# Kernel tuning notes

Hardware: AMD Instinct MI355X
Metric: run time of the kernel (lower is better)

Reference implementation:

```python
import jax, jax.numpy as jnp
import numpy as np

T, B, IN, H1, HB = 512, 256, 64, 128, 32  # seq, batch, input, LSTM width, bottleneck


def _lstm(x, w_ih, w_hh, b_ih, b_hh):
    """Single-layer unidirectional LSTM, time-major x: [T,B,in] -> [T,B,H].
    PyTorch gate order: i, f, g, o. Zero initial state."""
    H = w_hh.shape[1]
    # hoist input projection out of the scan: [T,B,4H]
    xg = jnp.einsum('tbi,gi->tbg', x, w_ih) + b_ih + b_hh

    def step(carry, xt):
        h, c = carry
        g = xt + h @ w_hh.T
        i, f, gg, o = jnp.split(g, 4, axis=-1)
        c = jax.nn.sigmoid(f) * c + jax.nn.sigmoid(i) * jnp.tanh(gg)
        h = jax.nn.sigmoid(o) * jnp.tanh(c)
        return (h, c), h

    h0 = jnp.zeros((x.shape[1], H), x.dtype)
    (_, _), hs = jax.lax.scan(step, (h0, h0), xg)
    return hs


def setup_inputs() -> dict:
    key = jax.random.key(0)
    ks = jax.random.split(key, 17)
    s = 0.05

    def p(k, shape):
        return jax.random.normal(k, shape, dtype=jnp.float32) * s

    return {
        'X': jax.random.normal(ks[0], (T, B, IN), dtype=jnp.float32),
        # en1: IN -> H1
        'w1_ih': p(ks[1], (4 * H1, IN)), 'w1_hh': p(ks[2], (4 * H1, H1)),
        'b1_ih': p(ks[3], (4 * H1,)), 'b1_hh': p(ks[4], (4 * H1,)),
        # en2: H1 -> HB
        'w2_ih': p(ks[5], (4 * HB, H1)), 'w2_hh': p(ks[6], (4 * HB, HB)),
        'b2_ih': p(ks[7], (4 * HB,)), 'b2_hh': p(ks[8], (4 * HB,)),
        # de1: HB -> H1
        'w3_ih': p(ks[9], (4 * H1, HB)), 'w3_hh': p(ks[10], (4 * H1, H1)),
        'b3_ih': p(ks[11], (4 * H1,)), 'b3_hh': p(ks[12], (4 * H1,)),
        # de2: H1 -> IN
        'w4_ih': p(ks[13], (4 * IN, H1)), 'w4_hh': p(ks[14], (4 * IN, IN)),
        'b4_ih': p(ks[15], (4 * IN,)), 'b4_hh': p(ks[16], (4 * IN,)),
    }


def reference(X, w1_ih, w1_hh, b1_ih, b1_hh, w2_ih, w2_hh, b2_ih, b2_hh,
              w3_ih, w3_hh, b3_ih, b3_hh, w4_ih, w4_hh, b4_ih, b4_hh):
    h = _lstm(X, w1_ih, w1_hh, b1_ih, b1_hh)      # [T,B,128]
    h = _lstm(h, w2_ih, w2_hh, b2_ih, b2_hh)      # [T,B,32]
    h = jnp.tanh(h)                               # bottleneck tanh
    h = _lstm(h, w3_ih, w3_hh, b3_ih, b3_hh)      # [T,B,128]
    out = _lstm(h, w4_ih, w4_hh, b4_ih, b4_hh)    # [T,B,64]
    return out
```

## Files before the change

### kernel.cpp

```cpp
#include <hip/hip_runtime.h>

#define T_STEPS 512
#define BATCH   256

typedef _Float16 f16;
typedef unsigned long long u64;
typedef __attribute__((ext_vector_type(8))) _Float16 f16x8;
typedef __attribute__((ext_vector_type(4))) _Float16 f16x4;
typedef __attribute__((ext_vector_type(4))) float    f32x4;

#define L2E 1.44269504088896340736f

__device__ __forceinline__ float rcp_f(float x)  { return __builtin_amdgcn_rcpf(x); }
__device__ __forceinline__ float exp2_f(float x) { return __builtin_amdgcn_exp2f(x); }

__device__ __forceinline__ float tanh_n(float x) {
    return fmaf(-2.0f, rcp_f(1.0f + exp2_f(2.0f * L2E * x)), 1.0f);
}
__device__ __forceinline__ u64 tanh4_f16(u64 v) {
    f16x4 h = __builtin_bit_cast(f16x4, v);
    f16x4 r;
#pragma unroll
    for (int i = 0; i < 4; ++i) r[i] = (f16)tanh_n((float)h[i]);
    return __builtin_bit_cast(u64, r);
}

__device__ __forceinline__ void barrier_lgkm() {
    asm volatile("s_waitcnt lgkmcnt(0)\n\ts_barrier" ::: "memory");
}
__device__ __forceinline__ void barrier_drain() {
    asm volatile("s_waitcnt vmcnt(0) lgkmcnt(0)\n\ts_barrier" ::: "memory");
}

__device__ __forceinline__ int  flag_load(const int* p) {
    return __hip_atomic_load(p, __ATOMIC_RELAXED, __HIP_MEMORY_SCOPE_AGENT);
}
__device__ __forceinline__ void flag_store(int* p, int v) {
    __hip_atomic_store(p, v, __ATOMIC_RELAXED, __HIP_MEMORY_SCOPE_AGENT);
}
__device__ __forceinline__ u64  panel_load(const u64* p) {
    return __hip_atomic_load(p, __ATOMIC_RELAXED, __HIP_MEMORY_SCOPE_AGENT);
}
__device__ __forceinline__ void panel_store(u64* p, u64 v) {
    __hip_atomic_store(p, v, __ATOMIC_RELAXED, __HIP_MEMORY_SCOPE_AGENT);
}

template <int IN_DIM, int H, bool IN_F32, bool OUT_PANEL, bool OUT_TANH>
__device__ __forceinline__ void lstm_layer_dev(
    char* sm,
    const void* __restrict__ xv,
    const int* in_flag,
    int* out_flag,
    const float* __restrict__ w_ih, const float* __restrict__ w_hh,
    const float* __restrict__ b_ih, const float* __restrict__ b_hh,
    void* __restrict__ outv,
    int group, int ltid)
{
    constexpr int KTX = IN_DIM / 32, KTH = H / 32, KT = KTX + KTH;
    constexpr int XP = IN_DIM + 8, HP = H + 8, NT = 4 * H;

    f16 (*xs)[16][XP] = (f16(*)[16][XP])sm;
    f16 (*hs)[16][HP] = (f16(*)[16][HP])(sm + 2 * 16 * XP * 2);

    const int wave = ltid >> 6, lane = ltid & 63;
    const int col = lane & 15, q = lane >> 4;
    const int bblk = group * 16;
    const int u = wave * 16 + col;

    f16x8 bw[4][KT];
#pragma unroll
    for (int g = 0; g < 4; ++g) {
        const float sc = (g == 2) ? 2.0f * L2E : L2E;
        const int row = g * H + u;
#pragma unroll
        for (int kt = 0; kt < KTX; ++kt) {
            const float* p = w_ih + (size_t)row * IN_DIM + kt * 32 + q * 8;
            f16x8 v;
#pragma unroll
            for (int j = 0; j < 8; ++j) v[j] = (f16)(p[j] * sc);
            bw[g][kt] = v;
        }
#pragma unroll
        for (int kt = 0; kt < KTH; ++kt) {
            const float* p = w_hh + (size_t)row * H + kt * 32 + q * 8;
            f16x8 v;
#pragma unroll
            for (int j = 0; j < 8; ++j) v[j] = (f16)(p[j] * sc);
            bw[g][KTX + kt] = v;
        }
    }
    float bias[4];
#pragma unroll
    for (int g = 0; g < 4; ++g)
        bias[g] = (b_ih[g * H + u] + b_hh[g * H + u]) * ((g == 2) ? 2.0f * L2E : L2E);
    float cst[4] = {0.f, 0.f, 0.f, 0.f};

    constexpr int ELD = IN_F32 ? 4 : 8;
    constexpr int EPR = IN_DIM / ELD;
    constexpr int NCH = 16 * EPR;
    constexpr int CPT = (NCH + NT - 1) / NT;
    constexpr long XADVB = (long)BATCH * IN_DIM * (IN_F32 ? 4 : 2);
    bool sv[CPT]; const char* sgp[CPT]; f16* slp[CPT];
    constexpr int LDSD = 16 * XP;
#pragma unroll
    for (int k = 0; k < CPT; ++k) {
        const int cc = ltid + k * NT;
        sv[k] = (cc < NCH);
        const int r_ = (cc < NCH ? cc : 0) / EPR;
        const int o_ = (cc < NCH ? cc : 0) % EPR;
        sgp[k] = (const char*)xv + ((size_t)(bblk + r_) * IN_DIM + o_ * ELD) * (IN_F32 ? 4 : 2);
        slp[k] = &xs[0][r_][o_ * ELD];
    }

    constexpr int OEPR = H / 4;
    u64* opg = nullptr;
    f16* olds = nullptr;
    float* outp_f32 = nullptr;
    if constexpr (OUT_PANEL) {
        const int orow = ltid / OEPR, ooff = ltid % OEPR;
        opg  = (u64*)((f16*)outv + (size_t)(bblk + orow) * H) + ooff;
        olds = &hs[0][orow][ooff * 4];
    } else {
        outp_f32 = (float*)outv + ((size_t)bblk + 4 * q) * H + u;
    }
    constexpr int HLDSD = 16 * HP;

    for (int i = ltid; i < 16 * HP; i += NT) hs[0][i / HP][i % HP] = (f16)0.f;
    int seen = 0;
    if constexpr (!IN_F32) {
        do { seen = flag_load(in_flag); } while (seen < 1);
    }
#pragma unroll
    for (int k = 0; k < CPT; ++k) {
        if (sv[k]) {
            if constexpr (IN_F32) {
                const f32x4 v = *reinterpret_cast<const f32x4*>(sgp[k]);
                f16x4 h4;
                h4[0] = (f16)v[0]; h4[1] = (f16)v[1]; h4[2] = (f16)v[2]; h4[3] = (f16)v[3];
                *reinterpret_cast<f16x4*>(slp[k]) = h4;
            } else {
                u64 a = panel_load((const u64*)sgp[k]);
                u64 b = panel_load((const u64*)sgp[k] + 1);
                u64 pk[2] = {a, b};
                *reinterpret_cast<f16x8*>(slp[k]) = *reinterpret_cast<const f16x8*>(pk);
            }
            sgp[k] += XADVB;
        }
    }
    barrier_drain();

    float hold[4] = {0.f, 0.f, 0.f, 0.f};

    auto step = [&](int t, int pbv, bool dodrain, bool dopub) {
        if constexpr (OUT_PANEL) {
            if (dopub && t >= 4 && ltid == 0) flag_store(out_flag, t - 1);
        }

        f32x4 xr32[CPT]; u64 xr16[CPT][2];
        const bool pf = (t + 1 < T_STEPS);
        if (pf) {
            if constexpr (!IN_F32) {
                if (seen < t + 2) {
                    do { seen = flag_load(in_flag); } while (seen < t + 2);
                }
            }
#pragma unroll
            for (int k = 0; k < CPT; ++k) {
                if (sv[k]) {
                    if constexpr (IN_F32) {
                        xr32[k] = *reinterpret_cast<const f32x4*>(sgp[k]);
                    } else {
                        xr16[k][0] = panel_load((const u64*)sgp[k]);
                        xr16[k][1] = panel_load((const u64*)sgp[k] + 1);
                    }
                    sgp[k] += XADVB;
                }
            }
        }

        if (t >= 1) {
            if constexpr (OUT_PANEL) {
                u64 v = *reinterpret_cast<const u64*>(olds + pbv * HLDSD);
                if constexpr (OUT_TANH) v = tanh4_f16(v);
                panel_store(opg, v);
                opg += (size_t)BATCH * H / 4;
            } else {
#pragma unroll
                for (int r = 0; r < 4; ++r) outp_f32[r * H] = hold[r];
                outp_f32 += (size_t)BATCH * H;
            }
        }

        f16x8 a[KT];
#pragma unroll
        for (int kt = 0; kt < KTX; ++kt)
            a[kt] = *reinterpret_cast<const f16x8*>(&xs[pbv][col][kt * 32 + q * 8]);
#pragma unroll
        for (int kt = 0; kt < KTH; ++kt)
            a[KTX + kt] = *reinterpret_cast<const f16x8*>(&hs[pbv][col][kt * 32 + q * 8]);

        f32x4 acc[4];
#pragma unroll
        for (int g = 0; g < 4; ++g)
            acc[g] = (f32x4){bias[g], bias[g], bias[g], bias[g]};
#pragma unroll
        for (int kt = 0; kt < KT; ++kt)
#pragma unroll
            for (int g = 0; g < 4; ++g)
                acc[g] = __builtin_amdgcn_mfma_f32_16x16x32_f16(a[kt], bw[g][kt], acc[g], 0, 0, 0);

#pragma unroll
        for (int r = 0; r < 4; ++r) {
            const float yi = acc[0][r];
            const float yf = acc[1][r];
            const float yg = acc[2][r];
            const float yo = acc[3][r];
            const float si = rcp_f(1.0f + exp2_f(-yi));
            const float sf = rcp_f(1.0f + exp2_f(-yf));
            const float dg = rcp_f(1.0f + exp2_f(yg));
            const float tgp = fmaf(dg, -4.0f * L2E, 2.0f * L2E);
            cst[r] = fmaf(sf, cst[r], si * tgp);
            const float dc = rcp_f(1.0f + exp2_f(cst[r]));
            const float th = fmaf(-2.0f, dc, 1.0f);
            const float so = rcp_f(1.0f + exp2_f(-yo));
            const float h = so * th;
            hs[pbv ^ 1][4 * q + r][u] = (f16)h;
            if constexpr (!OUT_PANEL) hold[r] = h;
        }

        if (pf) {
#pragma unroll
            for (int k = 0; k < CPT; ++k) {
                if (sv[k]) {
                    f16* dst = slp[k] + (pbv ^ 1) * LDSD;
                    if constexpr (IN_F32) {
                        f16x4 h4;
                        h4[0] = (f16)xr32[k][0]; h4[1] = (f16)xr32[k][1];
                        h4[2] = (f16)xr32[k][2]; h4[3] = (f16)xr32[k][3];
                        *reinterpret_cast<f16x4*>(dst) = h4;
                    } else {
                        *reinterpret_cast<f16x8*>(dst) =
                            *reinterpret_cast<const f16x8*>(xr16[k]);
                    }
                }
            }
        }

        if constexpr (!IN_F32) {
            if (dopub && seen < t + 9) seen = flag_load(in_flag);
        }

        if (dodrain) barrier_drain(); else barrier_lgkm();
    };

    for (int tb = 0; tb < T_STEPS; tb += 4) {
        step(tb + 0, 0, false, true);
        step(tb + 1, 1, false, false);
        step(tb + 2, 0, false, false);
        step(tb + 3, 1, true,  false);
    }

    if constexpr (OUT_PANEL) {
        u64 v = *reinterpret_cast<const u64*>(olds);
        if constexpr (OUT_TANH) v = tanh4_f16(v);
        panel_store(opg, v);
    } else {
#pragma unroll
        for (int r = 0; r < 4; ++r) outp_f32[r * H] = hold[r];
    }
    barrier_drain();
    if constexpr (OUT_PANEL) {
        if (ltid == 0) flag_store(out_flag, T_STEPS + 4);
    }
}

__global__ __launch_bounds__(512, 1)
void lstm_fused(const float* __restrict__ X,
                const float* __restrict__ w1_ih, const float* __restrict__ w1_hh,
                const float* __restrict__ b1_ih, const float* __restrict__ b1_hh,
                const float* __restrict__ w2_ih, const float* __restrict__ w2_hh,
                const float* __restrict__ b2_ih, const float* __restrict__ b2_hh,
                const float* __restrict__ w3_ih, const float* __restrict__ w3_hh,
                const float* __restrict__ b3_ih, const float* __restrict__ b3_hh,
                const float* __restrict__ w4_ih, const float* __restrict__ w4_hh,
                const float* __restrict__ b4_ih, const float* __restrict__ b4_hh,
                f16* __restrict__ h1, f16* __restrict__ h2, f16* __restrict__ h3,
                int* __restrict__ flags, float* __restrict__ out)
{
    __shared__ __attribute__((aligned(16))) char smem[45056];
    const int b = blockIdx.x, tid = threadIdx.x;

    if (b < 16) {
        lstm_layer_dev<64, 128, true, true, false>(
            smem, X, nullptr, flags + 0 * 16 + b,
            w1_ih, w1_hh, b1_ih, b1_hh, h1, b, tid);
    } else if (b < 20) {
        const int gl = tid >> 7;
        const int g  = (b - 16) * 4 + gl;
        lstm_layer_dev<128, 32, false, true, true>(
            smem + gl * 11264, h1, flags + 0 * 16 + g, flags + 1 * 16 + g,
            w2_ih, w2_hh, b2_ih, b2_hh, h2, g, tid & 127);
    } else if (b < 36) {
        const int g = b - 20;
        lstm_layer_dev<32, 128, false, true, false>(
            smem, h2, flags + 1 * 16 + g, flags + 2 * 16 + g,
            w3_ih, w3_hh, b3_ih, b3_hh, h3, g, tid);
    } else {
        const int gl = tid >> 8;
        const int g  = (b - 36) * 2 + gl;
        lstm_layer_dev<128, 64, false, false, false>(
            smem + gl * 13312, h3, flags + 2 * 16 + g, nullptr,
            w4_ih, w4_hh, b4_ih, b4_hh, out, g, tid & 255);
    }
}

extern "C" void kernel_launch(void* const* d_in, const int* in_sizes, int n_in,
                              void* d_out, int out_size, void* d_ws, size_t ws_size,
                              hipStream_t stream) {
    const float* X     = (const float*)d_in[0];
    const float* w1_ih = (const float*)d_in[1];
    const float* w1_hh = (const float*)d_in[2];
    const float* b1_ih = (const float*)d_in[3];
    const float* b1_hh = (const float*)d_in[4];
    const float* w2_ih = (const float*)d_in[5];
    const float* w2_hh = (const float*)d_in[6];
    const float* b2_ih = (const float*)d_in[7];
    const float* b2_hh = (const float*)d_in[8];
    const float* w3_ih = (const float*)d_in[9];
    const float* w3_hh = (const float*)d_in[10];
    const float* b3_ih = (const float*)d_in[11];
    const float* b3_hh = (const float*)d_in[12];
    const float* w4_ih = (const float*)d_in[13];
    const float* w4_hh = (const float*)d_in[14];
    const float* b4_ih = (const float*)d_in[15];
    const float* b4_hh = (const float*)d_in[16];

    float* out = (float*)d_out;

    int* flags = (int*)d_ws;
    f16* h1 = (f16*)((char*)d_ws + 256);
    f16* h2 = h1 + (size_t)T_STEPS * BATCH * 128;
    f16* h3 = h2 + (size_t)T_STEPS * BATCH * 32;

    lstm_fused<<<44, 512, 0, stream>>>(X,
        w1_ih, w1_hh, b1_ih, b1_hh, w2_ih, w2_hh, b2_ih, b2_hh,
        w3_ih, w3_hh, b3_ih, b3_hh, w4_ih, w4_hh, b4_ih, b4_hh,
        h1, h2, h3, flags, out);
}
```

Baseline: 650.7 us.

## Fuse LSTM layer pairs into shared-memory blocks, removing h1 and h3 global panels

Restructures the persistent kernel so that each block runs two LSTM layers together. Layers 1+2 share a block, with layer 2 reading layer 1's output from LDS in a software-pipelined, one-step-lagged schedule; layers 3+4 do the same. Only the bottleneck h2 crosses blocks through global memory with flags. This removes two global round trips and their flag spin-waits per step, and cuts the grid to 32 blocks of 768 threads. The cost is that a single block barrier now couples both layers' critical paths, so each step waits on the slower layer.

```diff
diff --git a/kernel.cpp b/kernel.cpp
--- a/kernel.cpp
+++ b/kernel.cpp
@@ -5,6 +5,7 @@
 
 typedef _Float16 f16;
 typedef unsigned long long u64;
+typedef unsigned int u32;
 typedef __attribute__((ext_vector_type(8))) _Float16 f16x8;
 typedef __attribute__((ext_vector_type(4))) _Float16 f16x4;
 typedef __attribute__((ext_vector_type(4))) float    f32x4;
@@ -45,160 +46,61 @@
     __hip_atomic_store(p, v, __ATOMIC_RELAXED, __HIP_MEMORY_SCOPE_AGENT);
 }
 
-template <int IN_DIM, int H, bool IN_F32, bool OUT_PANEL, bool OUT_TANH>
-__device__ __forceinline__ void lstm_layer_dev(
-    char* sm,
-    const void* __restrict__ xv,
-    const int* in_flag,
-    int* out_flag,
-    const float* __restrict__ w_ih, const float* __restrict__ w_hh,
-    const float* __restrict__ b_ih, const float* __restrict__ b_hh,
-    void* __restrict__ outv,
-    int group, int ltid)
-{
-    constexpr int KTX = IN_DIM / 32, KTH = H / 32, KT = KTX + KTH;
-    constexpr int XP = IN_DIM + 8, HP = H + 8, NT = 4 * H;
-
-    f16 (*xs)[16][XP] = (f16(*)[16][XP])sm;
-    f16 (*hs)[16][HP] = (f16(*)[16][HP])(sm + 2 * 16 * XP * 2);
-
-    const int wave = ltid >> 6, lane = ltid & 63;
-    const int col = lane & 15, q = lane >> 4;
-    const int bblk = group * 16;
-    const int u = wave * 16 + col;
-
+__device__ __forceinline__ void cvt_store4(f16* dst, f32x4 v) {
+    f16x4 h;
+    h[0] = (f16)v[0]; h[1] = (f16)v[1]; h[2] = (f16)v[2]; h[3] = (f16)v[3];
+    *reinterpret_cast<f16x4*>(dst) = h;
+}
+
+template <int IN_DIM, int H>
+struct Lstm {
+    static constexpr int KTX = IN_DIM / 32, KTH = H / 32, KT = KTX + KTH;
     f16x8 bw[4][KT];
-#pragma unroll
-    for (int g = 0; g < 4; ++g) {
-        const float sc = (g == 2) ? 2.0f * L2E : L2E;
-        const int row = g * H + u;
-#pragma unroll
-        for (int kt = 0; kt < KTX; ++kt) {
-            const float* p = w_ih + (size_t)row * IN_DIM + kt * 32 + q * 8;
-            f16x8 v;
-#pragma unroll
-            for (int j = 0; j < 8; ++j) v[j] = (f16)(p[j] * sc);
-            bw[g][kt] = v;
-        }
-#pragma unroll
-        for (int kt = 0; kt < KTH; ++kt) {
-            const float* p = w_hh + (size_t)row * H + kt * 32 + q * 8;
-            f16x8 v;
-#pragma unroll
-            for (int j = 0; j < 8; ++j) v[j] = (f16)(p[j] * sc);
-            bw[g][KTX + kt] = v;
+    float bias[4];
+    float cst[4];
+    int u, q;
+
+    __device__ __forceinline__ void init(const float* __restrict__ w_ih,
+                                         const float* __restrict__ w_hh,
+                                         const float* __restrict__ b_ih,
+                                         const float* __restrict__ b_hh,
+                                         int unit, int lane) {
+        q = lane >> 4;
+        u = unit * 16 + (lane & 15);
+#pragma unroll
+        for (int g = 0; g < 4; ++g) {
+            const float sc = (g == 2) ? 2.0f * L2E : L2E;
+            const int row = g * H + u;
+#pragma unroll
+            for (int kt = 0; kt < KTX; ++kt) {
+                const float* p = w_ih + (size_t)row * IN_DIM + kt * 32 + q * 8;
+                f16x8 v;
+#pragma unroll
+                for (int j = 0; j < 8; ++j) v[j] = (f16)(p[j] * sc);
+                bw[g][kt] = v;
+            }
+#pragma unroll
+            for (int kt = 0; kt < KTH; ++kt) {
+                const float* p = w_hh + (size_t)row * H + kt * 32 + q * 8;
+                f16x8 v;
+#pragma unroll
+                for (int j = 0; j < 8; ++j) v[j] = (f16)(p[j] * sc);
+                bw[g][KTX + kt] = v;
+            }
+            bias[g] = (b_ih[g * H + u] + b_hh[g * H + u]) * sc;
+            cst[g] = 0.f;
         }
     }
-    float bias[4];
-#pragma unroll
-    for (int g = 0; g < 4; ++g)
-        bias[g] = (b_ih[g * H + u] + b_hh[g * H + u]) * ((g == 2) ? 2.0f * L2E : L2E);
-    float cst[4] = {0.f, 0.f, 0.f, 0.f};
-
-    constexpr int ELD = IN_F32 ? 4 : 8;
-    constexpr int EPR = IN_DIM / ELD;
-    constexpr int NCH = 16 * EPR;
-    constexpr int CPT = (NCH + NT - 1) / NT;
-    constexpr long XADVB = (long)BATCH * IN_DIM * (IN_F32 ? 4 : 2);
-    bool sv[CPT]; const char* sgp[CPT]; f16* slp[CPT];
-    constexpr int LDSD = 16 * XP;
-#pragma unroll
-    for (int k = 0; k < CPT; ++k) {
-        const int cc = ltid + k * NT;
-        sv[k] = (cc < NCH);
-        const int r_ = (cc < NCH ? cc : 0) / EPR;
-        const int o_ = (cc < NCH ? cc : 0) % EPR;
-        sgp[k] = (const char*)xv + ((size_t)(bblk + r_) * IN_DIM + o_ * ELD) * (IN_F32 ? 4 : 2);
-        slp[k] = &xs[0][r_][o_ * ELD];
-    }
-
-    constexpr int OEPR = H / 4;
-    u64* opg = nullptr;
-    f16* olds = nullptr;
-    float* outp_f32 = nullptr;
-    if constexpr (OUT_PANEL) {
-        const int orow = ltid / OEPR, ooff = ltid % OEPR;
-        opg  = (u64*)((f16*)outv + (size_t)(bblk + orow) * H) + ooff;
-        olds = &hs[0][orow][ooff * 4];
-    } else {
-        outp_f32 = (float*)outv + ((size_t)bblk + 4 * q) * H + u;
-    }
-    constexpr int HLDSD = 16 * HP;
-
-    for (int i = ltid; i < 16 * HP; i += NT) hs[0][i / HP][i % HP] = (f16)0.f;
-    int seen = 0;
-    if constexpr (!IN_F32) {
-        do { seen = flag_load(in_flag); } while (seen < 1);
-    }
-#pragma unroll
-    for (int k = 0; k < CPT; ++k) {
-        if (sv[k]) {
-            if constexpr (IN_F32) {
-                const f32x4 v = *reinterpret_cast<const f32x4*>(sgp[k]);
-                f16x4 h4;
-                h4[0] = (f16)v[0]; h4[1] = (f16)v[1]; h4[2] = (f16)v[2]; h4[3] = (f16)v[3];
-                *reinterpret_cast<f16x4*>(slp[k]) = h4;
-            } else {
-                u64 a = panel_load((const u64*)sgp[k]);
-                u64 b = panel_load((const u64*)sgp[k] + 1);
-                u64 pk[2] = {a, b};
-                *reinterpret_cast<f16x8*>(slp[k]) = *reinterpret_cast<const f16x8*>(pk);
-            }
-            sgp[k] += XADVB;
-        }
-    }
-    barrier_drain();
-
-    float hold[4] = {0.f, 0.f, 0.f, 0.f};
-
-    auto step = [&](int t, int pbv, bool dodrain, bool dopub) {
-        if constexpr (OUT_PANEL) {
-            if (dopub && t >= 4 && ltid == 0) flag_store(out_flag, t - 1);
-        }
-
-        f32x4 xr32[CPT]; u64 xr16[CPT][2];
-        const bool pf = (t + 1 < T_STEPS);
-        if (pf) {
-            if constexpr (!IN_F32) {
-                if (seen < t + 2) {
-                    do { seen = flag_load(in_flag); } while (seen < t + 2);
-                }
-            }
-#pragma unroll
-            for (int k = 0; k < CPT; ++k) {
-                if (sv[k]) {
-                    if constexpr (IN_F32) {
-                        xr32[k] = *reinterpret_cast<const f32x4*>(sgp[k]);
-                    } else {
-                        xr16[k][0] = panel_load((const u64*)sgp[k]);
-                        xr16[k][1] = panel_load((const u64*)sgp[k] + 1);
-                    }
-                    sgp[k] += XADVB;
-                }
-            }
-        }
-
-        if (t >= 1) {
-            if constexpr (OUT_PANEL) {
-                u64 v = *reinterpret_cast<const u64*>(olds + pbv * HLDSD);
-                if constexpr (OUT_TANH) v = tanh4_f16(v);
-                panel_store(opg, v);
-                opg += (size_t)BATCH * H / 4;
-            } else {
-#pragma unroll
-                for (int r = 0; r < 4; ++r) outp_f32[r * H] = hold[r];
-                outp_f32 += (size_t)BATCH * H;
-            }
-        }
-
+
+    __device__ __forceinline__ void step(const f16* in_row, const f16* rec_row,
+                                         f16* hdst, int hp, float hold[4]) {
         f16x8 a[KT];
 #pragma unroll
         for (int kt = 0; kt < KTX; ++kt)
-            a[kt] = *reinterpret_cast<const f16x8*>(&xs[pbv][col][kt * 32 + q * 8]);
+            a[kt] = *reinterpret_cast<const f16x8*>(in_row + kt * 32 + q * 8);
 #pragma unroll
         for (int kt = 0; kt < KTH; ++kt)
-            a[KTX + kt] = *reinterpret_cast<const f16x8*>(&hs[pbv][col][kt * 32 + q * 8]);
-
+            a[KTX + kt] = *reinterpret_cast<const f16x8*>(rec_row + kt * 32 + q * 8);
         f32x4 acc[4];
 #pragma unroll
         for (int g = 0; g < 4; ++g)
@@ -208,13 +110,9 @@
 #pragma unroll
             for (int g = 0; g < 4; ++g)
                 acc[g] = __builtin_amdgcn_mfma_f32_16x16x32_f16(a[kt], bw[g][kt], acc[g], 0, 0, 0);
-
 #pragma unroll
         for (int r = 0; r < 4; ++r) {
-            const float yi = acc[0][r];
-            const float yf = acc[1][r];
-            const float yg = acc[2][r];
-            const float yo = acc[3][r];
+            const float yi = acc[0][r], yf = acc[1][r], yg = acc[2][r], yo = acc[3][r];
             const float si = rcp_f(1.0f + exp2_f(-yi));
             const float sf = rcp_f(1.0f + exp2_f(-yf));
             const float dg = rcp_f(1.0f + exp2_f(yg));
@@ -224,57 +122,13 @@
             const float th = fmaf(-2.0f, dc, 1.0f);
             const float so = rcp_f(1.0f + exp2_f(-yo));
             const float h = so * th;
-            hs[pbv ^ 1][4 * q + r][u] = (f16)h;
-            if constexpr (!OUT_PANEL) hold[r] = h;
-        }
-
-        if (pf) {
-#pragma unroll
-            for (int k = 0; k < CPT; ++k) {
-                if (sv[k]) {
-                    f16* dst = slp[k] + (pbv ^ 1) * LDSD;
-                    if constexpr (IN_F32) {
-                        f16x4 h4;
-                        h4[0] = (f16)xr32[k][0]; h4[1] = (f16)xr32[k][1];
-                        h4[2] = (f16)xr32[k][2]; h4[3] = (f16)xr32[k][3];
-                        *reinterpret_cast<f16x4*>(dst) = h4;
-                    } else {
-                        *reinterpret_cast<f16x8*>(dst) =
-                            *reinterpret_cast<const f16x8*>(xr16[k]);
-                    }
-                }
-            }
-        }
-
-        if constexpr (!IN_F32) {
-            if (dopub && seen < t + 9) seen = flag_load(in_flag);
-        }
-
-        if (dodrain) barrier_drain(); else barrier_lgkm();
-    };
-
-    for (int tb = 0; tb < T_STEPS; tb += 4) {
-        step(tb + 0, 0, false, true);
-        step(tb + 1, 1, false, false);
-        step(tb + 2, 0, false, false);
-        step(tb + 3, 1, true,  false);
+            hdst[(4 * q + r) * hp + u] = (f16)h;
+            hold[r] = h;
+        }
     }
-
-    if constexpr (OUT_PANEL) {
-        u64 v = *reinterpret_cast<const u64*>(olds);
-        if constexpr (OUT_TANH) v = tanh4_f16(v);
-        panel_store(opg, v);
-    } else {
-#pragma unroll
-        for (int r = 0; r < 4; ++r) outp_f32[r * H] = hold[r];
-    }
-    barrier_drain();
-    if constexpr (OUT_PANEL) {
-        if (ltid == 0) flag_store(out_flag, T_STEPS + 4);
-    }
-}
-
-__global__ __launch_bounds__(512, 1)
+};
+
+__global__ __launch_bounds__(768, 3)
 void lstm_fused(const float* __restrict__ X,
                 const float* __restrict__ w1_ih, const float* __restrict__ w1_hh,
                 const float* __restrict__ b1_ih, const float* __restrict__ b1_hh,
@@ -284,33 +138,226 @@
                 const float* __restrict__ b3_ih, const float* __restrict__ b3_hh,
                 const float* __restrict__ w4_ih, const float* __restrict__ w4_hh,
                 const float* __restrict__ b4_ih, const float* __restrict__ b4_hh,
-                f16* __restrict__ h1, f16* __restrict__ h2, f16* __restrict__ h3,
-                int* __restrict__ flags, float* __restrict__ out)
+                f16* __restrict__ h2t, int* __restrict__ flags,
+                float* __restrict__ out)
 {
-    __shared__ __attribute__((aligned(16))) char smem[45056];
+    __shared__ __attribute__((aligned(16))) char sm[16384];
     const int b = blockIdx.x, tid = threadIdx.x;
+    const int wave = tid >> 6, lane = tid & 63;
+    const int col = lane & 15;
 
     if (b < 16) {
-        lstm_layer_dev<64, 128, true, true, false>(
-            smem, X, nullptr, flags + 0 * 16 + b,
-            w1_ih, w1_hh, b1_ih, b1_hh, h1, b, tid);
-    } else if (b < 20) {
-        const int gl = tid >> 7;
-        const int g  = (b - 16) * 4 + gl;
-        lstm_layer_dev<128, 32, false, true, true>(
-            smem + gl * 11264, h1, flags + 0 * 16 + g, flags + 1 * 16 + g,
-            w2_ih, w2_hh, b2_ih, b2_hh, h2, g, tid & 127);
-    } else if (b < 36) {
-        const int g = b - 20;
-        lstm_layer_dev<32, 128, false, true, false>(
-            smem, h2, flags + 1 * 16 + g, flags + 2 * 16 + g,
-            w3_ih, w3_hh, b3_ih, b3_hh, h3, g, tid);
+        const int g = b, bblk = g * 16;
+        int* out_flag = flags + g;
+        constexpr int XP1 = 72, HP1 = 136, HP2 = 40;
+        constexpr int XS_P = 16 * XP1, H1_P = 16 * HP1, H2_P = 16 * HP2;
+        f16* xs  = (f16*)sm;
+        f16* h1  = (f16*)(sm + 4608);
+        f16* h2r = (f16*)(sm + 13312);
+
+        for (int i = tid; i < (2 * H1_P + 2 * H2_P) / 2; i += 768)
+            ((u32*)h1)[i] = 0u;
+
+        const float* xg0 = nullptr; const float* xg1 = nullptr;
+        f16* xl0 = nullptr; f16* xl1 = nullptr;
+        f32x4 hv0{}, hv1{};
+        if (wave >= 10) {
+            const int c0 = tid - 640, c1 = c0 + 128;
+            const int r0 = c0 >> 4, o0 = (c0 & 15) * 4;
+            const int r1 = c1 >> 4, o1 = (c1 & 15) * 4;
+            xg0 = X + (size_t)(bblk + r0) * 64 + o0;
+            xg1 = X + (size_t)(bblk + r1) * 64 + o1;
+            xl0 = xs + r0 * XP1 + o0;
+            xl1 = xs + r1 * XP1 + o1;
+            f32x4 v0 = *(const f32x4*)xg0, v1 = *(const f32x4*)xg1;
+            cvt_store4(xl0, v0); cvt_store4(xl1, v1);
+            xg0 += (size_t)BATCH * 64; xg1 += (size_t)BATCH * 64;
+            hv0 = *(const f32x4*)xg0; hv1 = *(const f32x4*)xg1;
+            xg0 += (size_t)BATCH * 64; xg1 += (size_t)BATCH * 64;
+        }
+        barrier_lgkm();
+
+        if (wave < 8) {
+            Lstm<64, 128> L;
+            L.init(w1_ih, w1_hh, b1_ih, b1_hh, wave, lane);
+            float hd[4];
+            const f16* in0 = xs + col * XP1;
+            const f16* in1 = xs + XS_P + col * XP1;
+            const f16* rc0 = h1 + col * HP1;
+            const f16* rc1 = h1 + H1_P + col * HP1;
+            f16* d0 = h1;
+            f16* d1 = h1 + H1_P;
+            for (int ss = 0; ss < 512; ss += 2) {
+                L.step(in0, rc1, d0, HP1, hd);
+                barrier_lgkm();
+                L.step(in1, rc0, d1, HP1, hd);
+                barrier_lgkm();
+            }
+            barrier_lgkm();
+            barrier_lgkm();
+        } else if (wave < 10) {
+            Lstm<128, 32> L;
+            L.init(w2_ih, w2_hh, b2_ih, b2_hh, wave - 8, lane);
+            float hd[4];
+            const int t2id = tid - 512, orow = t2id >> 3, ooff = t2id & 7;
+            u64* opg = (u64*)(h2t + (size_t)(bblk + orow) * 32) + ooff;
+            const f16* in0 = h1 + col * HP1;
+            const f16* in1 = h1 + H1_P + col * HP1;
+            const f16* rc0 = h2r + col * HP2;
+            const f16* rc1 = h2r + H2_P + col * HP2;
+            f16* d0 = h2r;
+            f16* d1 = h2r + H2_P;
+            const f16* ol0 = h2r + orow * HP2 + ooff * 4;
+            const f16* ol1 = h2r + H2_P + orow * HP2 + ooff * 4;
+            for (int ss = 0; ss < 512; ss += 2) {
+                if (ss >= 2) {
+                    panel_store(opg, tanh4_f16(*(const u64*)ol0));
+                    opg += (size_t)BATCH * 32 / 4;
+                    L.step(in1, rc0, d1, HP2, hd);
+                }
+                if (ss >= 4 && (ss & 3) == 0) barrier_drain(); else barrier_lgkm();
+                if (ss >= 4 && (ss & 3) == 0 && t2id == 0)
+                    flag_store(out_flag, ss - 1);
+                if (ss >= 2) {
+                    panel_store(opg, tanh4_f16(*(const u64*)ol1));
+                    opg += (size_t)BATCH * 32 / 4;
+                }
+                L.step(in0, rc1, d0, HP2, hd);
+                barrier_lgkm();
+            }
+            panel_store(opg, tanh4_f16(*(const u64*)ol0));
+            opg += (size_t)BATCH * 32 / 4;
+            L.step(in1, rc0, d1, HP2, hd);
+            barrier_lgkm();
+            panel_store(opg, tanh4_f16(*(const u64*)ol1));
+            barrier_drain();
+            if (t2id == 0) flag_store(out_flag, T_STEPS + 8);
+        } else {
+            for (int ss = 0; ss < 512; ss += 2) {
+                cvt_store4(xl0 + XS_P, hv0); cvt_store4(xl1 + XS_P, hv1);
+                if (ss + 2 < 512) {
+                    hv0 = *(const f32x4*)xg0; hv1 = *(const f32x4*)xg1;
+                    xg0 += (size_t)BATCH * 64; xg1 += (size_t)BATCH * 64;
+                }
+                barrier_lgkm();
+                if (ss + 2 < 512) { cvt_store4(xl0, hv0); cvt_store4(xl1, hv1); }
+                if (ss + 3 < 512) {
+                    hv0 = *(const f32x4*)xg0; hv1 = *(const f32x4*)xg1;
+                    xg0 += (size_t)BATCH * 64; xg1 += (size_t)BATCH * 64;
+                }
+                barrier_lgkm();
+            }
+            barrier_lgkm();
+            barrier_lgkm();
+        }
     } else {
-        const int gl = tid >> 8;
-        const int g  = (b - 36) * 2 + gl;
-        lstm_layer_dev<128, 64, false, false, false>(
-            smem + gl * 13312, h3, flags + 2 * 16 + g, nullptr,
-            w4_ih, w4_hh, b4_ih, b4_hh, out, g, tid & 255);
+        const int g = b - 16, bblk = g * 16;
+        const int* in_flag = flags + g;
+        constexpr int XP3 = 40, HP3 = 136, HP4 = 72;
+        constexpr int X3_P = 16 * XP3, H3_P = 16 * HP3, H4_P = 16 * HP4;
+        f16* xs3 = (f16*)sm;
+        f16* h3  = (f16*)(sm + 2560);
+        f16* h4  = (f16*)(sm + 11264);
+
+        for (int i = tid; i < (2 * H3_P + 2 * H4_P) / 2; i += 768)
+            ((u32*)h3)[i] = 0u;
+
+        const char* sgp = nullptr; f16* slp = nullptr;
+        u64 ha = 0, hb = 0;
+        int seen = 0;
+        if (wave == 0) {
+            const int r_ = tid >> 2, o_ = (tid & 3) * 8;
+            sgp = (const char*)h2t + ((size_t)(bblk + r_) * 32 + o_) * 2;
+            slp = xs3 + r_ * XP3 + o_;
+            do { seen = flag_load(in_flag); } while (seen < 1);
+            u64 pk[2];
+            pk[0] = panel_load((const u64*)sgp);
+            pk[1] = panel_load((const u64*)sgp + 1);
+            sgp += (size_t)BATCH * 64;
+            *reinterpret_cast<f16x8*>(slp) = *reinterpret_cast<const f16x8*>(pk);
+            while (seen < 2) seen = flag_load(in_flag);
+            ha = panel_load((const u64*)sgp);
+            hb = panel_load((const u64*)sgp + 1);
+            sgp += (size_t)BATCH * 64;
+        }
+        barrier_lgkm();
+
+        if (wave < 8) {
+            Lstm<32, 128> L;
+            L.init(w3_ih, w3_hh, b3_ih, b3_hh, wave, lane);
+            float hd[4];
+            const f16* in0 = xs3 + col * XP3;
+            const f16* in1 = xs3 + X3_P + col * XP3;
+            const f16* rc0 = h3 + col * HP3;
+            const f16* rc1 = h3 + H3_P + col * HP3;
+            f16* d0 = h3;
+            f16* d1 = h3 + H3_P;
+            for (int ss = 0; ss < 512; ss += 2) {
+                if (wave == 0) {
+                    u64 pk[2] = {ha, hb};
+                    *reinterpret_cast<f16x8*>(slp + X3_P) = *reinterpret_cast<const f16x8*>(pk);
+                    if (ss + 2 < 512) {
+                        if (seen < ss + 3) { do { seen = flag_load(in_flag); } while (seen < ss + 3); }
+                        ha = panel_load((const u64*)sgp);
+                        hb = panel_load((const u64*)sgp + 1);
+                        sgp += (size_t)BATCH * 64;
+                    }
+                }
+                L.step(in0, rc1, d0, HP3, hd);
+                barrier_lgkm();
+                if (wave == 0) {
+                    if (ss + 2 < 512) {
+                        u64 pk[2] = {ha, hb};
+                        *reinterpret_cast<f16x8*>(slp) = *reinterpret_cast<const f16x8*>(pk);
+                    }
+                    if (ss + 3 < 512) {
+                        if (seen < ss + 4) { do { seen = flag_load(in_flag); } while (seen < ss + 4); }
+                        ha = panel_load((const u64*)sgp);
+                        hb = panel_load((const u64*)sgp + 1);
+                        sgp += (size_t)BATCH * 64;
+                    }
+                }
+                L.step(in1, rc0, d1, HP3, hd);
+                barrier_lgkm();
+            }
+            barrier_lgkm();
+        } else {
+            Lstm<128, 64> L;
+            L.init(w4_ih, w4_hh, b4_ih, b4_hh, wave - 8, lane);
+            float hold[4] = {0.f, 0.f, 0.f, 0.f};
+            const int q4 = lane >> 4;
+            const int u4 = (wave - 8) * 16 + col;
+            float* outp = out + ((size_t)bblk + 4 * q4) * 64 + u4;
+            const f16* in0 = h3 + col * HP3;
+            const f16* in1 = h3 + H3_P + col * HP3;
+            const f16* rc0 = h4 + col * HP4;
+            const f16* rc1 = h4 + H4_P + col * HP4;
+            f16* d0 = h4;
+            f16* d1 = h4 + H4_P;
+            for (int ss = 0; ss < 512; ss += 2) {
+                if (ss >= 2) {
+#pragma unroll
+                    for (int r = 0; r < 4; ++r) outp[r * 64] = hold[r];
+                    outp += (size_t)BATCH * 64;
+                    L.step(in1, rc0, d1, HP4, hold);
+                }
+                barrier_lgkm();
+                if (ss >= 2) {
+#pragma unroll
+                    for (int r = 0; r < 4; ++r) outp[r * 64] = hold[r];
+                    outp += (size_t)BATCH * 64;
+                }
+                L.step(in0, rc1, d0, HP4, hold);
+                barrier_lgkm();
+            }
+#pragma unroll
+            for (int r = 0; r < 4; ++r) outp[r * 64] = hold[r];
+            outp += (size_t)BATCH * 64;
+            L.step(in1, rc0, d1, HP4, hold);
+            barrier_lgkm();
+#pragma unroll
+            for (int r = 0; r < 4; ++r) outp[r * 64] = hold[r];
+        }
     }
 }
 
@@ -338,12 +385,10 @@
     float* out = (float*)d_out;
 
     int* flags = (int*)d_ws;
-    f16* h1 = (f16*)((char*)d_ws + 256);
-    f16* h2 = h1 + (size_t)T_STEPS * BATCH * 128;
-    f16* h3 = h2 + (size_t)T_STEPS * BATCH * 32;
-
-    lstm_fused<<<44, 512, 0, stream>>>(X,
+    f16* h2t = (f16*)((char*)d_ws + 256);
+
+    lstm_fused<<<32, 768, 0, stream>>>(X,
         w1_ih, w1_hh, b1_ih, b1_hh, w2_ih, w2_hh, b2_ih, b2_hh,
         w3_ih, w3_hh, b3_ih, b3_hh, w4_ih, w4_hh, b4_ih, b4_hh,
-        h1, h2, h3, flags, out);
-}
+        h2t, flags, out);
+}
```

After: 721.1 us. 10.8% more time.
